# Kernel optimization log

Measured on AMD Instinct MI355X. Metric: run time of the kernel, lower is better.

Reference implementation:

```python
import jax, jax.numpy as jnp
import numpy as np

MARGIN = 0.3
B, D = 512, 128
NUM_CLASSES = 64


def setup_inputs() -> dict:
    key = jax.random.key(0)
    k1, k2 = jax.random.split(key)
    emb = jax.random.normal(k1, (B, D), dtype=jnp.float32)
    emb = emb / jnp.linalg.norm(emb, axis=-1, keepdims=True)  # docstring: L2-normalized
    labels = jax.random.randint(k2, (B,), 0, NUM_CLASSES, dtype=jnp.int64)
    return {"embeddings": emb, "labels": labels}


def reference(embeddings, labels):
    b = embeddings.shape[0]
    # pairwise euclidean distances (torch.cdist p=2)
    sq = jnp.sum(embeddings * embeddings, axis=-1)
    d2 = sq[:, None] + sq[None, :] - 2.0 * (embeddings @ embeddings.T)
    dist = jnp.sqrt(jnp.maximum(d2, 1e-12))  # [B, B]

    eq = labels[:, None] == labels[None, :]
    eye = jnp.eye(b, dtype=bool)
    pos_mask = eq & ~eye          # [i, p]
    neg_mask = ~eq                # [i, j]

    NEG_BIG = jnp.float32(-1e30)
    POS_BIG = jnp.float32(1e30)

    d_ap = dist[:, :, None]       # [i, p, 1]
    d_an = dist[:, None, :]       # [i, 1, j]
    # semi-hard: negative farther than positive but within margin
    semi = neg_mask[:, None, :] & (d_an > d_ap) & (d_an < d_ap + MARGIN)  # [i, p, j]
    semi_max = jnp.max(jnp.where(semi, d_an, NEG_BIG), axis=2)            # [i, p]
    has_semi = jnp.any(semi, axis=2)                                      # [i, p]
    # fallback: hardest (closest) negative per anchor
    min_neg = jnp.min(jnp.where(neg_mask, dist, POS_BIG), axis=1)         # [i]
    d_neg = jnp.where(has_semi, semi_max, min_neg[:, None])               # [i, p]

    has_neg = jnp.any(neg_mask, axis=1)
    valid = pos_mask & has_neg[:, None]

    per_pair = jax.nn.relu(dist - d_neg + MARGIN)
    total = jnp.sum(jnp.where(valid, per_pair, 0.0))
    cnt = jnp.sum(valid)
    return jnp.where(cnt > 0, total / jnp.maximum(cnt, 1).astype(total.dtype), jnp.float32(0.0))
```

## Files before the change

kernel.cpp:

```cpp
#include <hip/hip_runtime.h>

#define BN 512
#define DIM 128
#define TMARGIN 0.3f
#define NT 1024
#define NW 16
#define NBLK 256
#define BIGF 1e30f

#define FMA4(ACC, U, V)                                                \
    ACC.x += U.x * V.x; ACC.y += U.y * V.y;                            \
    ACC.z += U.z * V.z; ACC.w += U.w * V.w;

__device__ __forceinline__ float hsum4(float4 v) {
    return (v.x + v.y) + (v.z + v.w);
}

__global__ __launch_bounds__(NT, 4) void triplet_fused_kernel(
        const float* __restrict__ emb,
        const int* __restrict__ labels,
        float* __restrict__ psum,
        float* __restrict__ pcnt) {
    const int ia   = blockIdx.x;
    const int ib   = blockIdx.x + NBLK;
    const int tid  = threadIdx.x;
    const int lane = tid & 63;
    const int wave = tid >> 6;
    const int rl   = lane >> 2;
    const int kl   = lane & 3;

    __shared__ float drowA[BN], drowB[BN];
    __shared__ float pdA[BN], pdB[BN];
    __shared__ int   nposA, nposB;
    __shared__ float wsum[NW];
    __shared__ int   wcnt[NW];

    const float4* emb4 = (const float4*)emb;
    const int liA = labels[ia];
    const int liB = labels[ib];

    float4 ra[8], rb[8];
#pragma unroll
    for (int q = 0; q < 8; ++q) {
        ra[q] = emb4[(size_t)ia * 32 + kl + 4 * q];
        rb[q] = emb4[(size_t)ib * 32 + kl + 4 * q];
    }
    float4 sa = {0,0,0,0}, sb = {0,0,0,0};
#pragma unroll
    for (int q = 0; q < 8; ++q) { FMA4(sa, ra[q], ra[q]); FMA4(sb, rb[q], rb[q]); }
    float sqA = hsum4(sa), sqB = hsum4(sb);
    sqA += __shfl_xor(sqA, 1); sqA += __shfl_xor(sqA, 2);
    sqB += __shfl_xor(sqB, 1); sqB += __shfl_xor(sqB, 2);

    if (tid == 0) { nposA = 0; nposB = 0; }
    __syncthreads();

#pragma unroll
    for (int c = 0; c < 2; ++c) {
        const int r = c * 256 + wave * 16 + rl;
        float4 da = {0,0,0,0}, db = {0,0,0,0}, qq = {0,0,0,0};
#pragma unroll
        for (int q = 0; q < 8; ++q) {
            const float4 v = emb4[(size_t)r * 32 + kl + 4 * q];
            FMA4(da, ra[q], v);
            FMA4(db, rb[q], v);
            FMA4(qq, v, v);
        }
        float dotA = hsum4(da), dotB = hsum4(db), sqj = hsum4(qq);
        dotA += __shfl_down(dotA, 1); dotA += __shfl_down(dotA, 2);
        dotB += __shfl_down(dotB, 1); dotB += __shfl_down(dotB, 2);
        sqj  += __shfl_down(sqj, 1);  sqj  += __shfl_down(sqj, 2);
        if (kl == 0) {
            const int   lr = labels[r];
            const float dA = sqrtf(fmaxf(sqA + sqj - 2.f * dotA, 1e-12f));
            const float dB = sqrtf(fmaxf(sqB + sqj - 2.f * dotB, 1e-12f));
            const bool  eqA = (lr == liA), eqB = (lr == liB);
            drowA[r] = eqA ? BIGF : dA;
            drowB[r] = eqB ? BIGF : dB;
            if (eqA && r != ia) { int p = atomicAdd(&nposA, 1); pdA[p] = dA; }
            if (eqB && r != ib) { int p = atomicAdd(&nposB, 1); pdB[p] = dB; }
        }
    }
    __syncthreads();

    const int grp  = wave >> 3;
    const int wsub = wave & 7;
    const float* drow = grp ? drowB : drowA;
    const float* pd   = grp ? pdB   : pdA;
    const int    npos = grp ? nposB : nposA;

    float mn = BIGF;
#pragma unroll
    for (int kk = 0; kk < BN / 64; ++kk)
        mn = fminf(mn, drow[lane + 64 * kk]);
#pragma unroll
    for (int off = 32; off; off >>= 1)
        mn = fminf(mn, __shfl_xor(mn, off));

    float lsum = 0.f;
    int   lcnt = 0;
    if (mn < 1e29f) {
        for (int p = wsub; p < npos; p += 8) {
            const float dap = pd[p];
            const float hi  = dap + TMARGIN;
            float smax = -BIGF;
#pragma unroll
            for (int kk = 0; kk < BN / 64; ++kk) {
                const float dan = drow[lane + 64 * kk];
                if (dan > dap && dan < hi) smax = fmaxf(smax, dan);
            }
#pragma unroll
            for (int off = 32; off; off >>= 1)
                smax = fmaxf(smax, __shfl_xor(smax, off));
            const float dneg = (smax > -1e29f) ? smax : mn;
            lsum += fmaxf(dap - dneg + TMARGIN, 0.f);
            lcnt += 1;
        }
    }
    if (lane == 0) { wsum[wave] = lsum; wcnt[wave] = lcnt; }
    __syncthreads();

    if (tid == 0) {
        float s = 0.f;
        int   c = 0;
#pragma unroll
        for (int w = 0; w < NW; ++w) { s += wsum[w]; c += wcnt[w]; }
        psum[blockIdx.x] = s;
        pcnt[blockIdx.x] = (float)c;
    }
}

__global__ __launch_bounds__(64) void finalize_kernel(
        const float* __restrict__ psum,
        const float* __restrict__ pcnt,
        float* __restrict__ out) {
    const int lane = threadIdx.x;
    float s = 0.f, c = 0.f;
#pragma unroll
    for (int i = 0; i < 4; ++i) {
        s += psum[lane + 64 * i];
        c += pcnt[lane + 64 * i];
    }
#pragma unroll
    for (int off = 32; off; off >>= 1) {
        s += __shfl_xor(s, off);
        c += __shfl_xor(c, off);
    }
    if (lane == 0)
        out[0] = (c > 0.f) ? (s / fmaxf(c, 1.f)) : 0.f;
}

extern "C" void kernel_launch(void* const* d_in, const int* in_sizes, int n_in,
                              void* d_out, int out_size, void* d_ws, size_t ws_size,
                              hipStream_t stream) {
    const float* emb    = (const float*)d_in[0];
    const int*   labels = (const int*)d_in[1];
    float*       out    = (float*)d_out;
    float*       psum   = (float*)d_ws;
    float*       pcnt   = psum + NBLK;

    triplet_fused_kernel<<<NBLK, NT, 0, stream>>>(emb, labels, psum, pcnt);
    finalize_kernel<<<1, 64, 0, stream>>>(psum, pcnt, out);
}
```

Baseline: 63.87 us.

## Process four anchors per block with 8-lane dot products to halve grid

```diff
diff --git a/kernel.cpp b/kernel.cpp
--- a/kernel.cpp
+++ b/kernel.cpp
@@ -5,7 +5,7 @@
 #define TMARGIN 0.3f
 #define NT 1024
 #define NW 16
-#define NBLK 256
+#define NBLK 128
 #define BIGF 1e30f
 
 #define FMA4(ACC, U, V)                                                \
@@ -21,73 +21,101 @@
         const int* __restrict__ labels,
         float* __restrict__ psum,
         float* __restrict__ pcnt) {
-    const int ia   = blockIdx.x;
-    const int ib   = blockIdx.x + NBLK;
+    const int i0   = blockIdx.x;
+    const int i1   = blockIdx.x + 128;
+    const int i2   = blockIdx.x + 256;
+    const int i3   = blockIdx.x + 384;
     const int tid  = threadIdx.x;
     const int lane = tid & 63;
     const int wave = tid >> 6;
-    const int rl   = lane >> 2;
-    const int kl   = lane & 3;
+    const int rl   = lane >> 3;
+    const int kl   = lane & 7;
 
-    __shared__ float drowA[BN], drowB[BN];
-    __shared__ float pdA[BN], pdB[BN];
-    __shared__ int   nposA, nposB;
+    __shared__ float drows[4][BN];
+    __shared__ float pds[4][BN];
+    __shared__ int   nposArr[4];
     __shared__ float wsum[NW];
     __shared__ int   wcnt[NW];
 
     const float4* emb4 = (const float4*)emb;
-    const int liA = labels[ia];
-    const int liB = labels[ib];
+    const int li0 = labels[i0];
+    const int li1 = labels[i1];
+    const int li2 = labels[i2];
+    const int li3 = labels[i3];
 
-    float4 ra[8], rb[8];
+    float4 r0[4], r1[4], r2[4], r3[4];
 #pragma unroll
-    for (int q = 0; q < 8; ++q) {
-        ra[q] = emb4[(size_t)ia * 32 + kl + 4 * q];
-        rb[q] = emb4[(size_t)ib * 32 + kl + 4 * q];
+    for (int q = 0; q < 4; ++q) {
+        r0[q] = emb4[(size_t)i0 * 32 + kl + 8 * q];
+        r1[q] = emb4[(size_t)i1 * 32 + kl + 8 * q];
+        r2[q] = emb4[(size_t)i2 * 32 + kl + 8 * q];
+        r3[q] = emb4[(size_t)i3 * 32 + kl + 8 * q];
     }
-    float4 sa = {0,0,0,0}, sb = {0,0,0,0};
+    float4 s0 = {0,0,0,0}, s1 = {0,0,0,0}, s2 = {0,0,0,0}, s3 = {0,0,0,0};
 #pragma unroll
-    for (int q = 0; q < 8; ++q) { FMA4(sa, ra[q], ra[q]); FMA4(sb, rb[q], rb[q]); }
-    float sqA = hsum4(sa), sqB = hsum4(sb);
-    sqA += __shfl_xor(sqA, 1); sqA += __shfl_xor(sqA, 2);
-    sqB += __shfl_xor(sqB, 1); sqB += __shfl_xor(sqB, 2);
+    for (int q = 0; q < 4; ++q) {
+        FMA4(s0, r0[q], r0[q]); FMA4(s1, r1[q], r1[q]);
+        FMA4(s2, r2[q], r2[q]); FMA4(s3, r3[q], r3[q]);
+    }
+    float sq0 = hsum4(s0), sq1 = hsum4(s1), sq2 = hsum4(s2), sq3 = hsum4(s3);
+#pragma unroll
+    for (int off = 1; off < 8; off <<= 1) {
+        sq0 += __shfl_xor(sq0, off); sq1 += __shfl_xor(sq1, off);
+        sq2 += __shfl_xor(sq2, off); sq3 += __shfl_xor(sq3, off);
+    }
 
-    if (tid == 0) { nposA = 0; nposB = 0; }
+    if (tid < 4) nposArr[tid] = 0;
     __syncthreads();
 
 #pragma unroll
-    for (int c = 0; c < 2; ++c) {
-        const int r = c * 256 + wave * 16 + rl;
-        float4 da = {0,0,0,0}, db = {0,0,0,0}, qq = {0,0,0,0};
+    for (int c = 0; c < 4; ++c) {
+        const int r = c * 128 + wave * 8 + rl;
+        float4 d0 = {0,0,0,0}, d1 = {0,0,0,0};
+        float4 d2 = {0,0,0,0}, d3 = {0,0,0,0}, qq = {0,0,0,0};
 #pragma unroll
-        for (int q = 0; q < 8; ++q) {
-            const float4 v = emb4[(size_t)r * 32 + kl + 4 * q];
-            FMA4(da, ra[q], v);
-            FMA4(db, rb[q], v);
+        for (int q = 0; q < 4; ++q) {
+            const float4 v = emb4[(size_t)r * 32 + kl + 8 * q];
+            FMA4(d0, r0[q], v);
+            FMA4(d1, r1[q], v);
+            FMA4(d2, r2[q], v);
+            FMA4(d3, r3[q], v);
             FMA4(qq, v, v);
         }
-        float dotA = hsum4(da), dotB = hsum4(db), sqj = hsum4(qq);
-        dotA += __shfl_down(dotA, 1); dotA += __shfl_down(dotA, 2);
-        dotB += __shfl_down(dotB, 1); dotB += __shfl_down(dotB, 2);
-        sqj  += __shfl_down(sqj, 1);  sqj  += __shfl_down(sqj, 2);
+        float t0 = hsum4(d0), t1 = hsum4(d1);
+        float t2 = hsum4(d2), t3 = hsum4(d3), sqj = hsum4(qq);
+#pragma unroll
+        for (int off = 1; off < 8; off <<= 1) {
+            t0  += __shfl_down(t0, off);
+            t1  += __shfl_down(t1, off);
+            t2  += __shfl_down(t2, off);
+            t3  += __shfl_down(t3, off);
+            sqj += __shfl_down(sqj, off);
+        }
         if (kl == 0) {
             const int   lr = labels[r];
-            const float dA = sqrtf(fmaxf(sqA + sqj - 2.f * dotA, 1e-12f));
-            const float dB = sqrtf(fmaxf(sqB + sqj - 2.f * dotB, 1e-12f));
-            const bool  eqA = (lr == liA), eqB = (lr == liB);
-            drowA[r] = eqA ? BIGF : dA;
-            drowB[r] = eqB ? BIGF : dB;
-            if (eqA && r != ia) { int p = atomicAdd(&nposA, 1); pdA[p] = dA; }
-            if (eqB && r != ib) { int p = atomicAdd(&nposB, 1); pdB[p] = dB; }
+            const float dA = sqrtf(fmaxf(sq0 + sqj - 2.f * t0, 1e-12f));
+            const float dB = sqrtf(fmaxf(sq1 + sqj - 2.f * t1, 1e-12f));
+            const float dC = sqrtf(fmaxf(sq2 + sqj - 2.f * t2, 1e-12f));
+            const float dD = sqrtf(fmaxf(sq3 + sqj - 2.f * t3, 1e-12f));
+            const bool  e0 = (lr == li0), e1 = (lr == li1);
+            const bool  e2 = (lr == li2), e3 = (lr == li3);
+            drows[0][r] = e0 ? BIGF : dA;
+            drows[1][r] = e1 ? BIGF : dB;
+            drows[2][r] = e2 ? BIGF : dC;
+            drows[3][r] = e3 ? BIGF : dD;
+            if (e0 && r != i0) { int p = atomicAdd(&nposArr[0], 1); pds[0][p] = dA; }
+            if (e1 && r != i1) { int p = atomicAdd(&nposArr[1], 1); pds[1][p] = dB; }
+            if (e2 && r != i2) { int p = atomicAdd(&nposArr[2], 1); pds[2][p] = dC; }
+            if (e3 && r != i3) { int p = atomicAdd(&nposArr[3], 1); pds[3][p] = dD; }
         }
     }
     __syncthreads();
 
-    const int grp  = wave >> 3;
-    const int wsub = wave & 7;
-    const float* drow = grp ? drowB : drowA;
-    const float* pd   = grp ? pdB   : pdA;
-    const int    npos = grp ? nposB : nposA;
+    const int anc  = wave >> 2;
+    const int wsub = wave & 3;
+    const float* drow = drows[anc];
+    const float* pd   = pds[anc];
+    const int    npos = nposArr[anc];
 
     float mn = BIGF;
 #pragma unroll
@@ -100,7 +128,7 @@
     float lsum = 0.f;
     int   lcnt = 0;
     if (mn < 1e29f) {
-        for (int p = wsub; p < npos; p += 8) {
+        for (int p = wsub; p < npos; p += 4) {
             const float dap = pd[p];
             const float hi  = dap + TMARGIN;
             float smax = -BIGF;
@@ -137,7 +165,7 @@
     const int lane = threadIdx.x;
     float s = 0.f, c = 0.f;
 #pragma unroll
-    for (int i = 0; i < 4; ++i) {
+    for (int i = 0; i < NBLK / 64; ++i) {
         s += psum[lane + 64 * i];
         c += pcnt[lane + 64 * i];
     }
```

Result: slower. 65.88 us (+3.1%).
